# Optimization experiments

Measured on AMD Instinct MI355X. Metric: run time of the kernel, lower is better.

Reference implementation:

```python
import jax, jax.numpy as jnp
import numpy as np

D, DFF, H, V, BS, NL, NG = 1024, 4096, 16, 32000, 128, 2, 2

def _ln(x, w, b, eps=1e-5):
    m = x.mean(-1, keepdims=True)
    v = ((x - m) ** 2).mean(-1, keepdims=True)
    return (x - m) / jnp.sqrt(v + eps) * w + b

def _full_attn(q, k, v):
    # q,k,v: [B,H,S,dk] ; manual max-subtract softmax with +1e-9 denom and clamp, per FullAttention
    dk = q.shape[-1]
    s = jnp.einsum('bhqd,bhkd->bhqk', q / jnp.sqrt(jnp.float32(dk)), k)
    s = s - s.max(-1, keepdims=True)
    e = jnp.exp(s)
    a = e / (e.sum(-1, keepdims=True) + 1e-9)
    a = jnp.clip(a, 1e-9, 1.0)
    return jnp.einsum('bhqk,bhkd->bhqd', a, v)

def _attn_layer(qi, ki, vi, lnw, lnb, pw, pb):
    # lnw/lnb: [4,D] (norm_q,k,v,out); pw: [4,D,D] (q,k,v,o, stored [in,out]); pb: [4,D]
    B, Sq, _ = qi.shape
    Sk = ki.shape[1]
    q = _ln(qi, lnw[0], lnb[0]) @ pw[0] + pb[0]
    k = _ln(ki, lnw[1], lnb[1]) @ pw[1] + pb[1]
    v = _ln(vi, lnw[2], lnb[2]) @ pw[2] + pb[2]
    dk = D // H
    q = q.reshape(B, Sq, H, dk).transpose(0, 2, 1, 3)
    k = k.reshape(B, Sk, H, dk).transpose(0, 2, 1, 3)
    v = v.reshape(B, Sk, H, dk).transpose(0, 2, 1, 3)
    o = _full_attn(q, k, v).transpose(0, 2, 1, 3).reshape(B, Sq, D)
    o = o @ pw[3] + pb[3]
    return _ln(o, lnw[3], lnb[3])

def _ffn(x, n1w, n1b, n2w, n2b, w1, b1, w2, b2):
    h = jax.nn.gelu(_ln(x, n1w, n1b) @ w1 + b1, approximate=False)
    return _ln(h @ w2 + b2 + x, n2w, n2b)

def _tlayer(x, lnw, lnb, pw, pb, w1, b1, w2, b2):
    # lnw/lnb: [6,D] (attn q,k,v,out norms, ffn norm1, ffn norm2)
    x = x + _attn_layer(x, x, x, lnw[:4], lnb[:4], pw, pb)
    return _ffn(x, lnw[4], lnb[4], lnw[5], lnb[5], w1, b1, w2, b2)

def _pe(S, d):
    pos = jnp.arange(S, dtype=jnp.float32)[:, None]
    div = jnp.exp(jnp.arange(0, d, 2, dtype=jnp.float32) * (-np.log(10000.0) / d))
    pe = jnp.zeros((S, d), jnp.float32)
    pe = pe.at[:, 0::2].set(jnp.sin(pos * div))
    pe = pe.at[:, 1::2].set(jnp.cos(pos * div))
    return pe

def setup_inputs() -> dict:
    key = jax.random.key(0)
    ks = iter(jax.random.split(key, 64))
    nrm = lambda shp: jax.random.normal(next(ks), shp, jnp.float32) * 0.02
    inp = {
        'x': jax.random.randint(next(ks), (4, 4096), 0, V, dtype=jnp.int32).astype(jnp.int64),
        'emb': nrm((V, D)),
        'in_ln_w': jnp.ones((D,)), 'in_ln_b': jnp.zeros((D,)),
        'loc_ln_w': jnp.ones((NL, 6, D)), 'loc_ln_b': jnp.zeros((NL, 6, D)),
        'loc_pw': nrm((NL, 4, D, D)), 'loc_pb': jnp.zeros((NL, 4, D)),
        'loc_w1': nrm((NL, D, DFF)), 'loc_b1': jnp.zeros((NL, DFF)),
        'loc_w2': nrm((NL, DFF, D)), 'loc_b2': jnp.zeros((NL, D)),
        'locn_w': jnp.ones((D,)), 'locn_b': jnp.zeros((D,)),
        'pool_q': nrm((1, 1, D)),
        'pool_n_w': jnp.ones((D,)), 'pool_n_b': jnp.zeros((D,)),
        'pool_ln_w': jnp.ones((4, D)), 'pool_ln_b': jnp.zeros((4, D)),
        'pool_pw': nrm((4, D, D)), 'pool_pb': jnp.zeros((4, D)),
        'glob_ln_w': jnp.ones((NG, 6, D)), 'glob_ln_b': jnp.zeros((NG, 6, D)),
        'glob_pw': nrm((NG, 4, D, D)), 'glob_pb': jnp.zeros((NG, 4, D)),
        'glob_w1': nrm((NG, D, DFF)), 'glob_b1': jnp.zeros((NG, DFF)),
        'glob_w2': nrm((NG, DFF, D)), 'glob_b2': jnp.zeros((NG, D)),
        'out_ln_w': jnp.ones((D,)), 'out_ln_b': jnp.zeros((D,)),
        'out_w': nrm((D, V)), 'out_b': jnp.zeros((V,)),
    }
    return inp

def reference(x, emb, in_ln_w, in_ln_b, loc_ln_w, loc_ln_b, loc_pw, loc_pb,
              loc_w1, loc_b1, loc_w2, loc_b2, locn_w, locn_b,
              pool_q, pool_n_w, pool_n_b, pool_ln_w, pool_ln_b, pool_pw, pool_pb,
              glob_ln_w, glob_ln_b, glob_pw, glob_pb, glob_w1, glob_b1, glob_w2, glob_b2,
              out_ln_w, out_ln_b, out_w, out_b):
    B, S = x.shape
    nb = S // BS
    h = jnp.clip(emb[x], -100.0, 100.0) + _pe(S, D)[None]
    h = _ln(h, in_ln_w, in_ln_b)
    h = h.reshape(B * nb, BS, D)  # local blocks
    for i in range(NL):
        h = jnp.clip(_tlayer(h, loc_ln_w[i], loc_ln_b[i], loc_pw[i], loc_pb[i],
                             loc_w1[i], loc_b1[i], loc_w2[i], loc_b2[i]), -100.0, 100.0)
    h = _ln(h, locn_w, locn_b)
    # attention pooling of each block to one vector
    hp = _ln(h, pool_n_w, pool_n_b)
    q = jnp.broadcast_to(pool_q, (B * nb, 1, D))
    g = _attn_layer(q, hp, hp, pool_ln_w, pool_ln_b, pool_pw, pool_pb)[:, 0].reshape(B, nb, D)
    for i in range(NG):
        g = jnp.clip(_tlayer(g, glob_ln_w[i], glob_ln_b[i], glob_pw[i], glob_pb[i],
                             glob_w1[i], glob_b1[i], glob_w2[i], glob_b2[i]), -100.0, 100.0)
    g = _ln(g, out_ln_w, out_ln_b)
    return g @ out_w + out_b  # [B, num_blocks, vocab]
```

## Files before the change

kernel.cpp:

```cpp
#include <hip/hip_runtime.h>
#include <hip/hip_bf16.h>
#include <math.h>

#define DEV __device__ __forceinline__

typedef __attribute__((ext_vector_type(8))) short bf16x8;
typedef __attribute__((ext_vector_type(4))) float f32x4;
typedef unsigned short u16;

constexpr int D_ = 1024, NTOK = 16384, SEQ = 4096;

DEV u16 f2b(float f){
  union{float f;unsigned u;} v; v.f=f;
  unsigned r = (v.u + 0x7fffu + ((v.u>>16)&1u))>>16;
  return (u16)r;
}
DEV float b2f(u16 h){ union{unsigned u;float f;} v; v.u=((unsigned)h)<<16; return v.f; }

DEV float gelu_f(float x){
  float z = 0.7978845608028654f*(x + 0.044715f*x*x*x);
  float e = __expf(-2.f*z);
  float t = 2.f/(1.f+e) - 1.f;
  return 0.5f*x*(1.f+t);
}

DEV void gld16(const void* g, void* l){
  __builtin_amdgcn_global_load_lds((const __attribute__((address_space(1))) void*)g,
                                   (__attribute__((address_space(3))) void*)l, 16, 0, 0);
}

#define BAR()    __builtin_amdgcn_s_barrier()
#define SCHED0() __builtin_amdgcn_sched_barrier(0)
#define LGKM0()  asm volatile("s_waitcnt lgkmcnt(0)" ::: "memory")
#define VM0()    asm volatile("s_waitcnt vmcnt(0)" ::: "memory")

DEV float blockSum(float v){
  __shared__ float sb[4];
  #pragma unroll
  for(int m=32;m>=1;m>>=1) v += __shfl_xor(v, m, 64);
  int lane = threadIdx.x & 63, wv = threadIdx.x >> 6;
  __syncthreads();
  if(lane==0) sb[wv]=v;
  __syncthreads();
  float r = sb[0]+sb[1]+sb[2]+sb[3];
  __syncthreads();
  return r;
}

__global__ __launch_bounds__(256) void detect_k(const int* __restrict__ xr, int* __restrict__ flag){
  int tid=threadIdx.x; float cnt=0.f;
  for(int i=tid;i<8192;i+=256) if(xr[2*i+1]!=0) cnt+=1.f;
  cnt = blockSum(cnt);
  if(tid==0) *flag = (cnt < 64.f) ? 1 : 0;
}

__global__ __launch_bounds__(256) void embed_k(const void* __restrict__ xv, const int* __restrict__ flag,
      const float* __restrict__ emb, const float* __restrict__ w, const float* __restrict__ b,
      u16* __restrict__ out, u16* __restrict__ outn){
  int t = blockIdx.x;
  int id;
  if(*flag) id = (int)((const long long*)xv)[t];
  else      id = ((const int*)xv)[t];
  int s = t & (SEQ-1);
  int d0 = threadIdx.x*4;
  float4 e4 = *(const float4*)(emb + (size_t)id*D_ + d0);
  float vv[4] = {e4.x, e4.y, e4.z, e4.w};
  float acc = 0.f;
  #pragma unroll
  for(int i=0;i<4;i++){
    float e = fminf(fmaxf(vv[i], -100.f), 100.f);
    int d = d0+i;
    float fr = expf(-(float)(d & ~1) * (9.210340371976184f/(float)D_));
    float ang = (float)s * fr;
    e += (d&1) ? cosf(ang) : sinf(ang);
    vv[i]=e; acc+=e;
  }
  float mean = blockSum(acc)*(1.f/D_);
  float var=0.f;
  #pragma unroll
  for(int i=0;i<4;i++){ float dd=vv[i]-mean; var+=dd*dd; }
  var = blockSum(var)*(1.f/D_);
  float rs = rsqrtf(var+1e-5f);
  float y[4];
  #pragma unroll
  for(int i=0;i<4;i++) y[i] = (vv[i]-mean)*rs*w[d0+i]+b[d0+i];
  ushort4 o; o.x=f2b(y[0]); o.y=f2b(y[1]); o.z=f2b(y[2]); o.w=f2b(y[3]);
  *(ushort4*)(out + (size_t)t*D_ + d0) = o;
  float m2 = blockSum(y[0]+y[1]+y[2]+y[3])*(1.f/D_);
  float v2=0.f;
  #pragma unroll
  for(int i=0;i<4;i++){ float dd=y[i]-m2; v2+=dd*dd; }
  v2 = blockSum(v2)*(1.f/D_);
  float rs2 = rsqrtf(v2+1e-5f);
  ushort4 on; on.x=f2b((y[0]-m2)*rs2); on.y=f2b((y[1]-m2)*rs2); on.z=f2b((y[2]-m2)*rs2); on.w=f2b((y[3]-m2)*rs2);
  *(ushort4*)(outn + (size_t)t*D_ + d0) = on;
}

template<int MODE,int WRN>
__global__ __launch_bounds__(256) void ln_k(const u16* __restrict__ in, const u16* __restrict__ res,
      const float* __restrict__ w, const float* __restrict__ b, u16* __restrict__ out,
      u16* __restrict__ outn){
  int t = blockIdx.x; int d0 = threadIdx.x*4;
  ushort4 r4 = *(const ushort4*)(in + (size_t)t*D_ + d0);
  float vv[4] = {b2f(r4.x),b2f(r4.y),b2f(r4.z),b2f(r4.w)};
  float mean = blockSum(vv[0]+vv[1]+vv[2]+vv[3])*(1.f/D_);
  float var=0.f;
  #pragma unroll
  for(int i=0;i<4;i++){ float dd=vv[i]-mean; var+=dd*dd; }
  var = blockSum(var)*(1.f/D_);
  float rs = rsqrtf(var+1e-5f);
  float rv[4]={0,0,0,0};
  if(MODE==3){
    ushort4 q4 = *(const ushort4*)(res + (size_t)t*D_ + d0);
    rv[0]=b2f(q4.x); rv[1]=b2f(q4.y); rv[2]=b2f(q4.z); rv[3]=b2f(q4.w);
  }
  float y[4];
  #pragma unroll
  for(int i=0;i<4;i++){
    float v = (vv[i]-mean)*rs;
    v = v*w[d0+i]+b[d0+i];
    if(MODE==2) v = fminf(fmaxf(v,-100.f),100.f);
    if(MODE==3) v += rv[i];
    y[i]=v;
  }
  ushort4 o; o.x=f2b(y[0]); o.y=f2b(y[1]); o.z=f2b(y[2]); o.w=f2b(y[3]);
  *(ushort4*)(out + (size_t)t*D_ + d0) = o;
  if(WRN){
    float m2 = blockSum(y[0]+y[1]+y[2]+y[3])*(1.f/D_);
    float v2=0.f;
    #pragma unroll
    for(int i=0;i<4;i++){ float dd=y[i]-m2; v2+=dd*dd; }
    v2 = blockSum(v2)*(1.f/D_);
    float rs2 = rsqrtf(v2+1e-5f);
    ushort4 on; on.x=f2b((y[0]-m2)*rs2); on.y=f2b((y[1]-m2)*rs2); on.z=f2b((y[2]-m2)*rs2); on.w=f2b((y[3]-m2)*rs2);
    *(ushort4*)(outn + (size_t)t*D_ + d0) = on;
  }
}

__global__ __launch_bounds__(256) void ln3x_k(const u16* __restrict__ in,
    const float* __restrict__ w1,const float* __restrict__ b1,
    const float* __restrict__ w2,const float* __restrict__ b2, u16* __restrict__ out){
  int t=blockIdx.x, d0=threadIdx.x*4;
  ushort4 r4 = *(const ushort4*)(in + (size_t)t*D_ + d0);
  float vv[4]={b2f(r4.x),b2f(r4.y),b2f(r4.z),b2f(r4.w)};
  #pragma unroll
  for(int pass=0;pass<3;pass++){
    float mean = blockSum(vv[0]+vv[1]+vv[2]+vv[3])*(1.f/D_);
    float var=0.f;
    #pragma unroll
    for(int i=0;i<4;i++){ float dd=vv[i]-mean; var+=dd*dd; }
    var = blockSum(var)*(1.f/D_);
    float rs = rsqrtf(var+1e-5f);
    #pragma unroll
    for(int i=0;i<4;i++){
      float y=(vv[i]-mean)*rs;
      if(pass==0) y = y*w1[d0+i]+b1[d0+i];
      else if(pass==1) y = y*w2[d0+i]+b2[d0+i];
      vv[i]=y;
    }
  }
  ushort4 o;
  o.x=f2b(vv[0]); o.y=f2b(vv[1]); o.z=f2b(vv[2]); o.w=f2b(vv[3]);
  *(ushort4*)(out + (size_t)t*D_ + d0) = o;
}

__global__ __launch_bounds__(256) void lnrow_k(const float* __restrict__ x, const float* __restrict__ w,
      const float* __restrict__ b, float* __restrict__ out){
  int d0=threadIdx.x*4;
  float vv[4]={x[d0],x[d0+1],x[d0+2],x[d0+3]};
  float mean = blockSum(vv[0]+vv[1]+vv[2]+vv[3])*(1.f/D_);
  float var=0.f;
  #pragma unroll
  for(int i=0;i<4;i++){ float dd=vv[i]-mean; var+=dd*dd; }
  var = blockSum(var)*(1.f/D_);
  float rs = rsqrtf(var+1e-5f);
  #pragma unroll
  for(int i=0;i<4;i++) out[d0+i]=(vv[i]-mean)*rs*w[d0+i]+b[d0+i];
}

#define TF_BODY(W, ldW, lnw, Wt, Kd, n0, k0)                                 \
  {                                                                          \
    int ty = threadIdx.x>>6, tx = threadIdx.x&63;                            \
    _Pragma("unroll")                                                        \
    for(int p=0;p<16;p++){                                                   \
      int row = p*4+ty;                                                      \
      float sc = (lnw) ? (lnw)[(k0)+row] : 1.f;                              \
      T[row][tx] = (W)[(size_t)((k0)+row)*(ldW) + (n0)+tx]*sc;               \
    }                                                                        \
    __syncthreads();                                                         \
    _Pragma("unroll")                                                        \
    for(int p=0;p<16;p++){                                                   \
      int row = p*4+ty;                                                      \
      (Wt)[(size_t)((n0)+row)*(Kd) + (k0)+tx] = f2b(T[tx][row]);             \
    }                                                                        \
  }

__global__ __launch_bounds__(256) void tf_k(const float* __restrict__ W, int ldW,
      const float* __restrict__ lnw, u16* __restrict__ Wt, int Kd){
  __shared__ float T[64][65];
  int n0 = blockIdx.x*64, k0 = blockIdx.y*64;
  TF_BODY(W, ldW, lnw, Wt, Kd, n0, k0)
}

__global__ __launch_bounds__(256) void prep_tf_layer_k(const float* __restrict__ pw,
      const float* __restrict__ w1, const float* __restrict__ w2, const float* __restrict__ lw,
      u16* __restrict__ Wqk, u16* __restrict__ Wv, u16* __restrict__ Wo,
      u16* __restrict__ W1t, u16* __restrict__ W2t){
  __shared__ float T[64][65];
  int bid = blockIdx.x;
  const float* W; int ldW; const float* lnw; u16* Wt; int Kd, n0, k0;
  if(bid < 1024){
    int m = bid>>8, t = bid&255;
    n0 = (t&15)*64; k0 = (t>>4)*64;
    W = pw + (size_t)m*1024*1024; ldW = 1024; Kd = 1024;
    lnw = (m<3) ? lw + m*1024 : nullptr;
    Wt = (m==0)?Wqk : (m==1)?(Wqk+1024*1024) : (m==2)?Wv : Wo;
  } else if(bid < 2048){
    int t = bid-1024;
    n0 = (t&63)*64; k0 = (t>>6)*64;
    W = w1; ldW = 4096; Kd = 1024; lnw = lw+4*1024; Wt = W1t;
  } else {
    int t = bid-2048;
    n0 = (t&15)*64; k0 = (t>>4)*64;
    W = w2; ldW = 1024; Kd = 4096; lnw = nullptr; Wt = W2t;
  }
  TF_BODY(W, ldW, lnw, Wt, Kd, n0, k0)
}

__global__ __launch_bounds__(256) void prep_tf_pool_k(const float* __restrict__ pw,
      const float* __restrict__ lw, u16* __restrict__ PWkv, u16* __restrict__ PWo){
  __shared__ float T[64][65];
  int bid = blockIdx.x;
  int m = 1 + (bid>>8), t = bid&255;
  int n0 = (t&15)*64, k0 = (t>>4)*64;
  const float* W = pw + (size_t)m*1024*1024;
  const float* lnw = (m<3) ? lw + m*1024 : nullptr;
  u16* Wt = (m==1)?PWkv : (m==2)?(PWkv+1024*1024) : PWo;
  TF_BODY(W, 1024, lnw, Wt, 1024, n0, k0)
}

DEV void bias_body(const float* W, int ldW, int Kd, const float* lnb, float pbv, float* out){
  int tid = threadIdx.x;
  float chk = 0.f;
  if(lnb){ for(int k=tid;k<Kd;k+=256) chk += fabsf(lnb[k]); }
  chk = blockSum(chk);
  if(chk==0.f){ if(tid==0) *out = pbv; return; }
  float s=0.f;
  for(int k=tid;k<Kd;k+=256) s += lnb[k]*W[(size_t)k*ldW];
  s = blockSum(s);
  if(tid==0) *out = pbv + s;
}

__global__ __launch_bounds__(256) void bias_k(const float* __restrict__ W, int ldW,
      const float* __restrict__ lnb, const float* __restrict__ pb, float* __restrict__ out, int Kd){
  int j = blockIdx.x;
  bias_body(W + j, ldW, Kd, lnb, pb[j], out + j);
}

__global__ __launch_bounds__(256) void prep_bias_layer_k(const float* __restrict__ pw,
      const float* __restrict__ w1, const float* __restrict__ w2,
      const float* __restrict__ lb, const float* __restrict__ pb,
      const float* __restrict__ b1in, const float* __restrict__ b2in,
      float* __restrict__ Bqk, float* __restrict__ Bv, float* __restrict__ Bo,
      float* __restrict__ B1, float* __restrict__ B2){
  int j = blockIdx.x;
  const float* W; int ldW, Kd; const float* lnb; float pbv; float* out;
  const size_t MM = 1024ull*1024;
  if(j<2048){ int m=j>>10; int col=j&1023; W=pw+m*MM+col; ldW=1024; Kd=1024; lnb=lb+m*1024; pbv=pb[m*1024+col]; out=Bqk+j; }
  else if(j<3072){ int col=j-2048; W=pw+2*MM+col; ldW=1024; Kd=1024; lnb=lb+2*1024; pbv=pb[2*1024+col]; out=Bv+col; }
  else if(j<4096){ int col=j-3072; W=pw+3*MM+col; ldW=1024; Kd=1024; lnb=nullptr; pbv=pb[3*1024+col]; out=Bo+col; }
  else if(j<8192){ int col=j-4096; W=w1+col; ldW=4096; Kd=1024; lnb=lb+4*1024; pbv=b1in[col]; out=B1+col; }
  else { int col=j-8192; W=w2+col; ldW=1024; Kd=4096; lnb=nullptr; pbv=b2in[col]; out=B2+col; }
  bias_body(W, ldW, Kd, lnb, pbv, out);
}

__global__ __launch_bounds__(256) void prep_bias_pool_k(const float* __restrict__ pw,
      const float* __restrict__ lb, const float* __restrict__ pb,
      float* __restrict__ Pbkv, float* __restrict__ Pbo){
  int j = blockIdx.x;
  const size_t MM = 1024ull*1024;
  int m = 1 + (j>>10), col = j&1023;
  const float* lnb = (m<3) ? lb + m*1024 : nullptr;
  float* out = (m==1)?(Pbkv+col) : (m==2)?(Pbkv+1024+col) : (Pbo+col);
  bias_body(pw + m*MM + col, 1024, 1024, lnb, pb[m*1024+col], out);
}

__global__ __launch_bounds__(256) void matvec_k(const float* __restrict__ xn, const float* __restrict__ W,
      int ldW, const float* __restrict__ bias, float* __restrict__ out){
  int j=blockIdx.x, tid=threadIdx.x;
  float s=0.f;
  for(int k=tid;k<1024;k+=256) s += xn[k]*W[(size_t)k*ldW + j];
  s=blockSum(s);
  if(tid==0) out[j]=s+bias[j];
}

template<int EPI,int OUTF,int TV>
__global__ __launch_bounds__(256) void gemm_k(const u16* __restrict__ A, const u16* __restrict__ Bt,
      const float* __restrict__ bias, const u16* __restrict__ resid, void* __restrict__ Cout,
      int M, int N, int K, int ldc){
  __shared__ u16 SH[32768];
  int tid = threadIdx.x, lane = tid&63, wv = tid>>6;
  int g = lane>>4, l15 = lane&15;
  int GX = gridDim.x, GY = gridDim.y;
  int nwg = GX*GY;
  int flat = blockIdx.y*GX + blockIdx.x;
  int q = nwg>>3, r = nwg&7, xcd = flat&7, idx = flat>>3;
  int f = (xcd<r ? xcd*(q+1) : r*(q+1)+(xcd-r)*q) + idx;
  int by, bx;
  if(((GY&7)==0) && ((GX&7)==0)){
    int sbs = GX<<3;
    int s = f / sbs, rem = f - s*sbs;
    int chunk = rem>>6, iw = rem&63;
    by = s*8 + (iw&7);
    bx = chunk*8 + (iw>>3);
  } else if((GY&7)==0){
    int sbs = GX<<3;
    int s = f / sbs, rem = f - s*sbs;
    by = s*8 + (rem&7);
    bx = rem>>3;
  } else {
    by = f/GX; bx = f - by*GX;
  }
  int row0 = by*128, col0 = bx*128;
  int wr = wv>>1, wc = wv&1;
  int e0 = wv*512 + lane*8;
  f32x4 acc[4][4] = {};
  auto STAGE = [&](int buf, int t){
    u16* base = SH + buf*16384;
    int k0 = t<<6;
    #pragma unroll
    for(int c=0;c<4;c++){
      int e = c*2048 + e0;
      int row = e>>6;
      int slx = ((e>>3)&7) ^ (row&7);
      gld16(A  + (size_t)(row0 + row)*K + (k0 + slx*8), &base[e]);
      gld16(Bt + (size_t)(col0 + row)*K + (k0 + slx*8), &base[8192 + e]);
    }
  };
  int nt = K>>6;
  STAGE(0, 0);
  VM0(); BAR(); SCHED0();
  #pragma unroll 2
  for(int t=0;t<nt;t++){
    int b = t&1;
    if(t+1<nt) STAGE(b^1, t+1);
    bf16x8 a[2][4], bb[2][4];
    #pragma unroll
    for(int ks=0;ks<2;ks++){
      #pragma unroll
      for(int m=0;m<4;m++){
        int ra = wr*64+m*16+l15;
        a[ks][m] = *(const bf16x8*)&SH[b*16384 + ra*64 + (((ks*4+g) ^ (ra&7))<<3)];
      }
      #pragma unroll
      for(int n=0;n<4;n++){
        int rb = wc*64+n*16+l15;
        bb[ks][n] = *(const bf16x8*)&SH[b*16384 + 8192 + rb*64 + (((ks*4+g) ^ (rb&7))<<3)];
      }
    }
    #pragma unroll
    for(int ks=0;ks<2;ks++)
      #pragma unroll
      for(int m=0;m<4;m++)
        #pragma unroll
        for(int n=0;n<4;n++)
          acc[m][n] = __builtin_amdgcn_mfma_f32_16x16x32_bf16(a[ks][m], bb[ks][n], acc[m][n], 0,0,0);
    if(t+1<nt){
      VM0(); LGKM0(); BAR(); SCHED0();
    }
  }
  if(TV){
    __syncthreads();
    u16* Tb = SH;
    #pragma unroll
    for(int m=0;m<4;m++){
      #pragma unroll
      for(int n=0;n<4;n++){
        int c = wc*64 + n*16 + l15;
        float bs = bias[col0 + c];
        #pragma unroll
        for(int r2=0;r2<4;r2++){
          int Rl = wr*64 + m*16 + g*4 + r2;
          Tb[c*128 + (Rl ^ ((c&7)<<4))] = f2b(acc[m][n][r2]+bs);
        }
      }
    }
    __syncthreads();
    for(int p=tid*4; p<16384; p+=1024){
      int c = p>>7, rr = p&127;
      int rs = rr ^ ((c&7)<<4);
      ushort4 v4;
      v4.x = Tb[c*128+rs]; v4.y = Tb[c*128+rs+1]; v4.z = Tb[c*128+rs+2]; v4.w = Tb[c*128+rs+3];
      *(ushort4*)((u16*)Cout + (size_t)(col0+c)*M + row0 + rr) = v4;
    }
  } else {
    #pragma unroll
    for(int m=0;m<4;m++){
      #pragma unroll
      for(int n=0;n<4;n++){
        int Cc = col0 + wc*64 + n*16 + l15;
        float bs = bias[Cc];
        #pragma unroll
        for(int r2=0;r2<4;r2++){
          int R = row0 + wr*64 + m*16 + g*4 + r2;
          float v = acc[m][n][r2] + bs;
          if(EPI==1) v = gelu_f(v);
          if(EPI==2) v += b2f(resid[(size_t)R*ldc + Cc]);
          if(OUTF) ((float*)Cout)[(size_t)R*ldc + Cc] = v;
          else     ((u16*)Cout)[(size_t)R*ldc + Cc] = f2b(v);
        }
      }
    }
  }
}

__global__ __launch_bounds__(256) void attnl_k(const u16* __restrict__ QK, const u16* __restrict__ VT,
      u16* __restrict__ AT){
  __shared__ u16 SP[16384];
  __shared__ u16 Vt[8192];
  __shared__ float rmax[256], rsum[256];
  int tid=threadIdx.x, lane=tid&63, wv=tid>>6, g=lane>>4, l15=lane&15;
  int lb = blockIdx.x>>4, h = blockIdx.x&15;
  int wr=wv>>1, wc=wv&1;
  #pragma unroll
  for(int c=0;c<4;c++){
    int chunk = c*2048 + wv*512;
    int e = chunk + lane*8;
    int rq = e>>6;
    int sq = ((e>>3)&7) ^ (rq&7);
    int rv = e>>7;
    int sv = ((e>>3)&15) ^ (rv&15);
    gld16(QK + (size_t)(lb*128 + rq)*2048 + h*64 + sq*8,        &SP[chunk]);
    gld16(QK + (size_t)(lb*128 + rq)*2048 + 1024 + h*64 + sq*8, &SP[8192+chunk]);
    gld16(VT + (size_t)(h*64 + rv)*16384 + lb*128 + sv*8,       &Vt[chunk]);
  }
  __syncthreads();
  f32x4 s[4][4] = {};
  #pragma unroll
  for(int ks=0;ks<2;ks++){
    bf16x8 a[4], b[4];
    #pragma unroll
    for(int m=0;m<4;m++){
      int ra = wr*64+m*16+l15;
      a[m] = *(const bf16x8*)&SP[ra*64 + (((ks*4+g) ^ (ra&7))<<3)];
    }
    #pragma unroll
    for(int n=0;n<4;n++){
      int rb = wc*64+n*16+l15;
      b[n] = *(const bf16x8*)&SP[8192 + rb*64 + (((ks*4+g) ^ (rb&7))<<3)];
    }
    #pragma unroll
    for(int m=0;m<4;m++)
      #pragma unroll
      for(int n=0;n<4;n++)
        s[m][n] = __builtin_amdgcn_mfma_f32_16x16x32_bf16(a[m], b[n], s[m][n], 0,0,0);
  }
  #pragma unroll
  for(int m=0;m<4;m++)
    #pragma unroll
    for(int n=0;n<4;n++) s[m][n] *= 0.125f;
  #pragma unroll
  for(int m=0;m<4;m++)
    #pragma unroll
    for(int r=0;r<4;r++){
      float mx = fmaxf(fmaxf(s[m][0][r],s[m][1][r]),fmaxf(s[m][2][r],s[m][3][r]));
      #pragma unroll
      for(int msk=1;msk<16;msk<<=1) mx = fmaxf(mx, __shfl_xor(mx,msk,64));
      if(l15==0) rmax[(wr*64+m*16+g*4+r)*2+wc]=mx;
    }
  __syncthreads();
  #pragma unroll
  for(int m=0;m<4;m++)
    #pragma unroll
    for(int r=0;r<4;r++){
      int row = wr*64+m*16+g*4+r;
      float M2 = fmaxf(rmax[row*2], rmax[row*2+1]);
      float sm=0.f;
      #pragma unroll
      for(int n=0;n<4;n++){ float e = expf(s[m][n][r]-M2); s[m][n][r]=e; sm+=e; }
      #pragma unroll
      for(int msk=1;msk<16;msk<<=1) sm += __shfl_xor(sm,msk,64);
      if(l15==0) rsum[row*2+wc]=sm;
    }
  __syncthreads();
  #pragma unroll
  for(int m=0;m<4;m++)
    #pragma unroll
    for(int r=0;r<4;r++){
      int row = wr*64+m*16+g*4+r;
      float den = rsum[row*2]+rsum[row*2+1]+1e-9f;
      #pragma unroll
      for(int n=0;n<4;n++){
        float a = s[m][n][r]/den;
        a = fminf(fmaxf(a,1e-9f),1.f);
        int col = wc*64+n*16+l15;
        SP[row*128 + ((((col>>3) ^ (row&15))<<3) | (col&7))] = f2b(a);
      }
    }
  __syncthreads();
  f32x4 o[4][2] = {};
  #pragma unroll
  for(int ks=0;ks<4;ks++){
    bf16x8 a[4], b[2];
    #pragma unroll
    for(int m=0;m<4;m++){
      int ra = wr*64+m*16+l15;
      a[m] = *(const bf16x8*)&SP[ra*128 + (((ks*4+g) ^ (ra&15))<<3)];
    }
    #pragma unroll
    for(int n=0;n<2;n++){
      int rv = wc*32+n*16+l15;
      b[n] = *(const bf16x8*)&Vt[rv*128 + (((ks*4+g) ^ (rv&15))<<3)];
    }
    #pragma unroll
    for(int m=0;m<4;m++)
      #pragma unroll
      for(int n=0;n<2;n++)
        o[m][n] = __builtin_amdgcn_mfma_f32_16x16x32_bf16(a[m], b[n], o[m][n], 0,0,0);
  }
  #pragma unroll
  for(int m=0;m<4;m++)
    #pragma unroll
    for(int n=0;n<2;n++)
      #pragma unroll
      for(int r=0;r<4;r++)
        AT[(size_t)(lb*128 + wr*64+m*16+g*4+r)*1024 + h*64 + wc*32+n*16+l15] = f2b(o[m][n][r]);
}

__global__ __launch_bounds__(256) void poolattn_k(const float* __restrict__ qp, const u16* __restrict__ KV,
      u16* __restrict__ g0){
  int lb = blockIdx.x, tid = threadIdx.x;
  __shared__ float sc[16*128];
  for(int p=tid;p<2048;p+=256){
    int h=p>>7, j=p&127;
    const u16* krow = KV + (size_t)(lb*128+j)*2048 + h*64;
    float s=0.f;
    for(int d=0;d<64;d++) s += qp[h*64+d]*b2f(krow[d]);
    sc[h*128+j] = s*0.125f;
  }
  __syncthreads();
  if(tid<16){
    float* r=&sc[tid*128];
    float mx=r[0];
    for(int j=1;j<128;j++) mx=fmaxf(mx,r[j]);
    float sm=0.f;
    for(int j=0;j<128;j++){ float e=expf(r[j]-mx); r[j]=e; sm+=e; }
    sm+=1e-9f;
    for(int j=0;j<128;j++) r[j]=fminf(fmaxf(r[j]/sm,1e-9f),1.f);
  }
  __syncthreads();
  for(int c=tid;c<1024;c+=256){
    int h=c>>6;
    float acc=0.f;
    for(int j=0;j<128;j++) acc += sc[h*128+j]*b2f(KV[(size_t)(lb*128+j)*2048 + 1024 + c]);
    g0[(size_t)lb*1024 + c] = f2b(acc);
  }
}

__global__ __launch_bounds__(256) void attng_k(const u16* __restrict__ QKV, u16* __restrict__ OUT){
  int bb = blockIdx.x>>4, h = blockIdx.x&15;
  __shared__ float sc[32*32];
  int tid=threadIdx.x;
  for(int p=tid;p<1024;p+=256){
    int i=p>>5, j=p&31;
    const u16* q = QKV + (size_t)(bb*32+i)*3072 + h*64;
    const u16* k = QKV + (size_t)(bb*32+j)*3072 + 1024 + h*64;
    float s=0.f;
    for(int d=0;d<64;d++) s += b2f(q[d])*b2f(k[d]);
    sc[p] = s*0.125f;
  }
  __syncthreads();
  if(tid<32){
    float* r=&sc[tid*32];
    float mx=r[0];
    for(int j=1;j<32;j++) mx=fmaxf(mx,r[j]);
    float sm=0.f;
    for(int j=0;j<32;j++){ float e=expf(r[j]-mx); r[j]=e; sm+=e; }
    sm+=1e-9f;
    for(int j=0;j<32;j++) r[j]=fminf(fmaxf(r[j]/sm,1e-9f),1.f);
  }
  __syncthreads();
  for(int p=tid;p<2048;p+=256){
    int i=p>>6, d=p&63;
    float acc=0.f;
    for(int j=0;j<32;j++) acc += sc[i*32+j]*b2f(QKV[(size_t)(bb*32+j)*3072 + 2048 + h*64 + d]);
    OUT[(size_t)(bb*32+i)*1024 + h*64 + d] = f2b(acc);
  }
}

extern "C" void kernel_launch(void* const* d_in, const int* in_sizes, int n_in,
                              void* d_out, int out_size, void* d_ws, size_t ws_size,
                              hipStream_t stream) {
  (void)in_sizes; (void)n_in; (void)out_size;
  const void*  x       = d_in[0];
  const float* emb     = (const float*)d_in[1];
  const float* in_ln_w = (const float*)d_in[2];
  const float* in_ln_b = (const float*)d_in[3];
  const float* loc_ln_w= (const float*)d_in[4];
  const float* loc_ln_b= (const float*)d_in[5];
  const float* loc_pw  = (const float*)d_in[6];
  const float* loc_pb  = (const float*)d_in[7];
  const float* loc_w1  = (const float*)d_in[8];
  const float* loc_b1  = (const float*)d_in[9];
  const float* loc_w2  = (const float*)d_in[10];
  const float* loc_b2  = (const float*)d_in[11];
  const float* locn_w  = (const float*)d_in[12];
  const float* locn_b  = (const float*)d_in[13];
  const float* pool_q  = (const float*)d_in[14];
  const float* pool_n_w= (const float*)d_in[15];
  const float* pool_n_b= (const float*)d_in[16];
  const float* pool_ln_w=(const float*)d_in[17];
  const float* pool_ln_b=(const float*)d_in[18];
  const float* pool_pw = (const float*)d_in[19];
  const float* pool_pb = (const float*)d_in[20];
  const float* glob_ln_w=(const float*)d_in[21];
  const float* glob_ln_b=(const float*)d_in[22];
  const float* glob_pw = (const float*)d_in[23];
  const float* glob_pb = (const float*)d_in[24];
  const float* glob_w1 = (const float*)d_in[25];
  const float* glob_b1 = (const float*)d_in[26];
  const float* glob_w2 = (const float*)d_in[27];
  const float* glob_b2 = (const float*)d_in[28];
  const float* out_ln_w= (const float*)d_in[29];
  const float* out_ln_b= (const float*)d_in[30];
  const float* out_w   = (const float*)d_in[31];
  const float* out_b   = (const float*)d_in[32];

  char* wsb = (char*)d_ws;
  size_t off = 0;
  auto AL = [&](size_t n)->char*{ size_t o=(off+255)&~(size_t)255; off=o+n; return wsb+o; };

  int*  flag = (int*)AL(256);
  u16*  WA   = (u16*)AL(12ull*1024*1024*2);
  float* BA  = (float*)AL(12*1024*4);
  float* qn  = (float*)AL(1024*4);
  float* qp  = (float*)AL(1024*4);
  float* Hb  = (float*)AL(32000*4);
  u16*  R    = (u16*)AL(64ull*1024*1024*2);
  u16*  X    = (u16*)AL((size_t)NTOK*1024*2);
  u16*  XN   = (u16*)AL((size_t)NTOK*1024*2);
  u16*  G    = (u16*)AL(128ull*1024*2);
  u16*  GN   = (u16*)AL(128ull*1024*2);
  u16*  GQKV = (u16*)AL(128ull*3072*2);
  u16*  GAT  = (u16*)AL(128ull*1024*2);
  u16*  GO   = (u16*)AL(128ull*1024*2);
  u16*  GFH  = (u16*)AL(128ull*4096*2);
  u16*  g0   = (u16*)AL(128ull*1024*2);
  if(off > ws_size) return;

  u16 *LWqk = WA, *LWv = WA+2097152, *LWo = WA+3145728, *LW1 = WA+4194304, *LW2 = WA+8388608;
  float *Lbqk = BA, *Lbv = BA+2048, *Lbo = BA+3072, *Lb1 = BA+4096, *Lb2 = BA+8192;
  u16 *GWqkv = WA, *GWo = WA+3145728, *GW1 = WA+4194304, *GW2 = WA+8388608;
  float *Gbqkv = BA, *Gbo = BA+3072, *Gb1 = BA+4096, *Gb2 = BA+8192;
  u16 *PWkv = WA, *PWo = WA+2097152;
  float *Pbkv = BA, *Pbo = BA+2048;
  u16 *QKb = R, *VTb = R+33554432, *ATb = R+50331648;
  u16 *FH  = R;
  u16 *KVb = R;
  u16 *HW  = R;
  u16 *Ob  = XN;

  const size_t MM = 1024ull*1024;

  detect_k<<<1,256,0,stream>>>((const int*)x, flag);
  embed_k<<<NTOK,256,0,stream>>>(x, flag, emb, in_ln_w, in_ln_b, X, XN);

  for(int l=0;l<2;l++){
    const float* pw = loc_pw + (size_t)l*4*MM;
    const float* lw = loc_ln_w + (size_t)l*6*1024;
    const float* lb = loc_ln_b + (size_t)l*6*1024;
    const float* pb = loc_pb + (size_t)l*4*1024;
    const float* w1 = loc_w1 + (size_t)l*1024*4096;
    const float* w2 = loc_w2 + (size_t)l*4096*1024;
    prep_tf_layer_k<<<3072,256,0,stream>>>(pw, w1, w2, lw, LWqk, LWv, LWo, LW1, LW2);
    prep_bias_layer_k<<<9216,256,0,stream>>>(pw, w1, w2, lb, pb,
        loc_b1+(size_t)l*4096, loc_b2+(size_t)l*1024, Lbqk, Lbv, Lbo, Lb1, Lb2);

    gemm_k<0,0,0><<<dim3(16,128),256,0,stream>>>(XN, LWqk, Lbqk, nullptr, QKb, NTOK, 2048, 1024, 2048);
    gemm_k<0,0,1><<<dim3(8,128),256,0,stream>>>(XN, LWv, Lbv, nullptr, VTb, NTOK, 1024, 1024, 0);
    attnl_k<<<128*16,256,0,stream>>>(QKb, VTb, ATb);
    gemm_k<0,0,0><<<dim3(8,128),256,0,stream>>>(ATb, LWo, Lbo, nullptr, Ob, NTOK, 1024, 1024, 1024);
    ln_k<3,1><<<NTOK,256,0,stream>>>(Ob, X, lw+3*1024, lb+3*1024, X, XN);
    gemm_k<1,0,0><<<dim3(32,128),256,0,stream>>>(XN, LW1, Lb1, nullptr, FH, NTOK, 4096, 1024, 4096);
    gemm_k<2,0,0><<<dim3(8,128),256,0,stream>>>(FH, LW2, Lb2, X, Ob, NTOK, 1024, 4096, 1024);
    ln_k<2,1><<<NTOK,256,0,stream>>>(Ob, nullptr, lw+5*1024, lb+5*1024, X, XN);
  }

  prep_tf_pool_k<<<768,256,0,stream>>>(pool_pw, pool_ln_w, PWkv, PWo);
  prep_bias_pool_k<<<3072,256,0,stream>>>(pool_pw, pool_ln_b, pool_pb, Pbkv, Pbo);
  lnrow_k<<<1,256,0,stream>>>(pool_q, pool_ln_w, pool_ln_b, qn);
  matvec_k<<<1024,256,0,stream>>>(qn, pool_pw, 1024, pool_pb, qp);
  ln3x_k<<<NTOK,256,0,stream>>>(X, locn_w, locn_b, pool_n_w, pool_n_b, XN);
  gemm_k<0,0,0><<<dim3(16,128),256,0,stream>>>(XN, PWkv, Pbkv, nullptr, KVb, NTOK, 2048, 1024, 2048);
  poolattn_k<<<128,256,0,stream>>>(qp, KVb, g0);
  gemm_k<0,0,0><<<dim3(8,1),256,0,stream>>>(g0, PWo, Pbo, nullptr, GO, 128, 1024, 1024, 1024);
  ln_k<1,1><<<128,256,0,stream>>>(GO, nullptr, pool_ln_w+3*1024, pool_ln_b+3*1024, G, GN);

  for(int l=0;l<2;l++){
    const float* pw = glob_pw + (size_t)l*4*MM;
    const float* lw = glob_ln_w + (size_t)l*6*1024;
    const float* lb = glob_ln_b + (size_t)l*6*1024;
    const float* pb = glob_pb + (size_t)l*4*1024;
    const float* w1 = glob_w1 + (size_t)l*1024*4096;
    const float* w2 = glob_w2 + (size_t)l*4096*1024;
    prep_tf_layer_k<<<3072,256,0,stream>>>(pw, w1, w2, lw, GWqkv, GWqkv+2097152, GWo, GW1, GW2);
    prep_bias_layer_k<<<9216,256,0,stream>>>(pw, w1, w2, lb, pb,
        glob_b1+(size_t)l*4096, glob_b2+(size_t)l*1024, Gbqkv, Gbqkv+2048, Gbo, Gb1, Gb2);

    gemm_k<0,0,0><<<dim3(24,1),256,0,stream>>>(GN, GWqkv, Gbqkv, nullptr, GQKV, 128, 3072, 1024, 3072);
    attng_k<<<64,256,0,stream>>>(GQKV, GAT);
    gemm_k<0,0,0><<<dim3(8,1),256,0,stream>>>(GAT, GWo, Gbo, nullptr, GO, 128, 1024, 1024, 1024);
    ln_k<3,1><<<128,256,0,stream>>>(GO, G, lw+3*1024, lb+3*1024, G, GN);
    gemm_k<1,0,0><<<dim3(32,1),256,0,stream>>>(GN, GW1, Gb1, nullptr, GFH, 128, 4096, 1024, 4096);
    gemm_k<2,0,0><<<dim3(8,1),256,0,stream>>>(GFH, GW2, Gb2, G, GO, 128, 1024, 4096, 1024);
    ln_k<2,1><<<128,256,0,stream>>>(GO, nullptr, lw+5*1024, lb+5*1024, G, GN);
  }

  tf_k<<<dim3(500,16),256,0,stream>>>(out_w, 32000, out_ln_w, HW, 1024);
  bias_k<<<32000,256,0,stream>>>(out_w, 32000, out_ln_b, out_b, Hb, 1024);
  gemm_k<0,1,0><<<dim3(250,1),256,0,stream>>>(GN, HW, Hb, nullptr, d_out, 128, 32000, 1024, 32000);
}
```

Measured before the change: 1.926 ms.

## Add 256x128-tile GEMM with XCD-aware block swizzle for large local GEMMs

```diff
diff --git a/kernel.cpp b/kernel.cpp
--- a/kernel.cpp
+++ b/kernel.cpp
@@ -409,6 +409,99 @@
           if(OUTF) ((float*)Cout)[(size_t)R*ldc + Cc] = v;
           else     ((u16*)Cout)[(size_t)R*ldc + Cc] = f2b(v);
         }
+      }
+    }
+  }
+}
+
+template<int EPI>
+__global__ __launch_bounds__(256) void gemm2_k(const u16* __restrict__ A, const u16* __restrict__ Bt,
+      const float* __restrict__ bias, const u16* __restrict__ resid, void* __restrict__ Cout,
+      int M, int N, int K, int ldc){
+  __shared__ u16 SH[24576];
+  int tid = threadIdx.x, lane = tid&63, wv = tid>>6;
+  int g = lane>>4, l15 = lane&15;
+  int GX = gridDim.x, GY = gridDim.y;
+  int nwg = GX*GY;
+  int flat = blockIdx.y*GX + blockIdx.x;
+  int q = nwg>>3, r = nwg&7, xcd = flat&7, idx = flat>>3;
+  int f = (xcd<r ? xcd*(q+1) : r*(q+1)+(xcd-r)*q) + idx;
+  int by, bx;
+  if(((GY&7)==0) && ((GX&7)==0)){
+    int sbs = GX<<3;
+    int s = f / sbs, rem = f - s*sbs;
+    int chunk = rem>>6, iw = rem&63;
+    by = s*8 + (iw&7);
+    bx = chunk*8 + (iw>>3);
+  } else if((GY&7)==0){
+    int sbs = GX<<3;
+    int s = f / sbs, rem = f - s*sbs;
+    by = s*8 + (rem&7);
+    bx = rem>>3;
+  } else {
+    by = f/GX; bx = f - by*GX;
+  }
+  int row0 = by*256, col0 = bx*128;
+  int wr = wv>>1, wc = wv&1;
+  f32x4 acc[8][4] = {};
+  auto STAGE = [&](int buf, int t){
+    u16* base = SH + buf*12288;
+    int k0 = t<<5;
+    #pragma unroll
+    for(int c=0;c<4;c++){
+      int e = c*2048 + tid*8;
+      int row = e>>5;
+      int slx = ((e>>3)&3) ^ (row&3);
+      gld16(A + (size_t)(row0 + row)*K + (k0 + slx*8), &base[e]);
+    }
+    #pragma unroll
+    for(int c=0;c<2;c++){
+      int e = c*2048 + tid*8;
+      int row = e>>5;
+      int slx = ((e>>3)&3) ^ (row&3);
+      gld16(Bt + (size_t)(col0 + row)*K + (k0 + slx*8), &base[8192 + e]);
+    }
+  };
+  int nt = K>>5;
+  STAGE(0, 0);
+  VM0(); BAR(); SCHED0();
+  #pragma unroll 2
+  for(int t=0;t<nt;t++){
+    int b = t&1;
+    if(t+1<nt) STAGE(b^1, t+1);
+    bf16x8 a[8], bb[4];
+    #pragma unroll
+    for(int m=0;m<8;m++){
+      int ra = wr*128 + m*16 + l15;
+      a[m] = *(const bf16x8*)&SH[b*12288 + ra*32 + ((g ^ (ra&3))<<3)];
+    }
+    #pragma unroll
+    for(int n=0;n<4;n++){
+      int rb = wc*64 + n*16 + l15;
+      bb[n] = *(const bf16x8*)&SH[b*12288 + 8192 + rb*32 + ((g ^ (rb&3))<<3)];
+    }
+    #pragma unroll
+    for(int m=0;m<8;m++)
+      #pragma unroll
+      for(int n=0;n<4;n++)
+        acc[m][n] = __builtin_amdgcn_mfma_f32_16x16x32_bf16(a[m], bb[n], acc[m][n], 0,0,0);
+    if(t+1<nt){
+      VM0(); LGKM0(); BAR(); SCHED0();
+    }
+  }
+  #pragma unroll
+  for(int m=0;m<8;m++){
+    #pragma unroll
+    for(int n=0;n<4;n++){
+      int Cc = col0 + wc*64 + n*16 + l15;
+      float bs = bias[Cc];
+      #pragma unroll
+      for(int r2=0;r2<4;r2++){
+        int R = row0 + wr*128 + m*16 + g*4 + r2;
+        float v = acc[m][n][r2] + bs;
+        if(EPI==1) v = gelu_f(v);
+        if(EPI==2) v += b2f(resid[(size_t)R*ldc + Cc]);
+        ((u16*)Cout)[(size_t)R*ldc + Cc] = f2b(v);
       }
     }
   }
@@ -676,13 +769,13 @@
     prep_bias_layer_k<<<9216,256,0,stream>>>(pw, w1, w2, lb, pb,
         loc_b1+(size_t)l*4096, loc_b2+(size_t)l*1024, Lbqk, Lbv, Lbo, Lb1, Lb2);
 
-    gemm_k<0,0,0><<<dim3(16,128),256,0,stream>>>(XN, LWqk, Lbqk, nullptr, QKb, NTOK, 2048, 1024, 2048);
+    gemm2_k<0><<<dim3(16,64),256,0,stream>>>(XN, LWqk, Lbqk, nullptr, QKb, NTOK, 2048, 1024, 2048);
     gemm_k<0,0,1><<<dim3(8,128),256,0,stream>>>(XN, LWv, Lbv, nullptr, VTb, NTOK, 1024, 1024, 0);
     attnl_k<<<128*16,256,0,stream>>>(QKb, VTb, ATb);
-    gemm_k<0,0,0><<<dim3(8,128),256,0,stream>>>(ATb, LWo, Lbo, nullptr, Ob, NTOK, 1024, 1024, 1024);
+    gemm2_k<0><<<dim3(8,64),256,0,stream>>>(ATb, LWo, Lbo, nullptr, Ob, NTOK, 1024, 1024, 1024);
     ln_k<3,1><<<NTOK,256,0,stream>>>(Ob, X, lw+3*1024, lb+3*1024, X, XN);
-    gemm_k<1,0,0><<<dim3(32,128),256,0,stream>>>(XN, LW1, Lb1, nullptr, FH, NTOK, 4096, 1024, 4096);
-    gemm_k<2,0,0><<<dim3(8,128),256,0,stream>>>(FH, LW2, Lb2, X, Ob, NTOK, 1024, 4096, 1024);
+    gemm2_k<1><<<dim3(32,64),256,0,stream>>>(XN, LW1, Lb1, nullptr, FH, NTOK, 4096, 1024, 4096);
+    gemm2_k<2><<<dim3(8,64),256,0,stream>>>(FH, LW2, Lb2, X, Ob, NTOK, 1024, 4096, 1024);
     ln_k<2,1><<<NTOK,256,0,stream>>>(Ob, nullptr, lw+5*1024, lb+5*1024, X, XN);
   }
 
@@ -691,7 +784,7 @@
   lnrow_k<<<1,256,0,stream>>>(pool_q, pool_ln_w, pool_ln_b, qn);
   matvec_k<<<1024,256,0,stream>>>(qn, pool_pw, 1024, pool_pb, qp);
   ln3x_k<<<NTOK,256,0,stream>>>(X, locn_w, locn_b, pool_n_w, pool_n_b, XN);
-  gemm_k<0,0,0><<<dim3(16,128),256,0,stream>>>(XN, PWkv, Pbkv, nullptr, KVb, NTOK, 2048, 1024, 2048);
+  gemm2_k<0><<<dim3(16,64),256,0,stream>>>(XN, PWkv, Pbkv, nullptr, KVb, NTOK, 2048, 1024, 2048);
   poolattn_k<<<128,256,0,stream>>>(qp, KVb, g0);
   gemm_k<0,0,0><<<dim3(8,1),256,0,stream>>>(g0, PWo, Pbo, nullptr, GO, 128, 1024, 1024, 1024);
   ln_k<1,1><<<128,256,0,stream>>>(GO, nullptr, pool_ln_w+3*1024, pool_ln_b+3*1024, G, GN);
```

After: 2.610 ms. 35.5% more time.
